# Optimization experiments

Measured on AMD Instinct MI355X. Metric: run time of the kernel, lower is better.

The kernel has to match this reference:

```python
import jax, jax.numpy as jnp
import numpy as np

N_NODES = 50000
N_EDGES = 800000
N_FEAT = 128
HIDDEN = 128
HEADS = 4
C = HIDDEN // HEADS  # per-head channels = 32
N_LAYERS = 3
OUT_DIM = 2048
N_GRAPHS = 1000
LEAKY = 0.2  # PyG GATConv default negative_slope


def setup_inputs() -> dict:
    key = jax.random.key(0)
    ks = jax.random.split(key, 12)
    x = jax.random.normal(ks[0], (N_NODES, N_FEAT), dtype=jnp.float32)
    edge_index = jax.random.randint(ks[1], (2, N_EDGES), 0, N_NODES, dtype=jnp.int32)
    edge_attr = jax.random.normal(ks[2], (N_EDGES, 1), dtype=jnp.float32)
    batch = (jnp.arange(N_NODES, dtype=jnp.int32) // (N_NODES // N_GRAPHS))  # 50 nodes per graph
    s = 1.0 / np.sqrt(HIDDEN)
    Ws = jax.random.normal(ks[3], (N_LAYERS, N_FEAT, HIDDEN), dtype=jnp.float32) * s
    att_src = jax.random.normal(ks[4], (N_LAYERS, HEADS, C), dtype=jnp.float32) * s
    att_dst = jax.random.normal(ks[5], (N_LAYERS, HEADS, C), dtype=jnp.float32) * s
    We = jax.random.normal(ks[6], (N_LAYERS, 1, HIDDEN), dtype=jnp.float32) * s
    att_e = jax.random.normal(ks[7], (N_LAYERS, HEADS, C), dtype=jnp.float32) * s
    biases = jnp.zeros((N_LAYERS, HIDDEN), dtype=jnp.float32)
    lin1_w = jax.random.normal(ks[8], (HIDDEN, OUT_DIM), dtype=jnp.float32) * s
    lin1_b = jnp.zeros((OUT_DIM,), dtype=jnp.float32)
    return {"x": x, "edge_index": edge_index, "edge_attr": edge_attr, "batch": batch,
            "Ws": Ws, "att_src": att_src, "att_dst": att_dst, "We": We,
            "att_e": att_e, "biases": biases, "lin1_w": lin1_w, "lin1_b": lin1_b}


def _gat_layer(x, src, dst, ea, W, a_s, a_d, We_l, a_e, b):
    """PyG GATConv: shared lin for src/dst, edge_dim=1, concat heads, eval mode."""
    N = x.shape[0]
    h = (x @ W).reshape(N, HEADS, C)                       # [N,H,C]
    al_s = jnp.einsum('nhc,hc->nh', h, a_s)                # [N,H]
    al_d = jnp.einsum('nhc,hc->nh', h, a_d)
    e = (ea @ We_l).reshape(-1, HEADS, C)                  # [E',H,C]
    al_e = jnp.einsum('ehc,hc->eh', e, a_e)
    logits = jax.nn.leaky_relu(al_s[src] + al_d[dst] + al_e, LEAKY)  # [E',H]
    # segment softmax over incoming edges of each dst node, per head
    m = jax.ops.segment_max(logits, dst, num_segments=N)
    m = jnp.where(jnp.isfinite(m), m, 0.0)
    ex = jnp.exp(logits - m[dst])
    den = jax.ops.segment_sum(ex, dst, num_segments=N)
    alpha = ex / (den[dst] + 1e-16)                        # [E',H]
    msg = alpha[:, :, None] * h[src]                       # [E',H,C]
    out = jax.ops.segment_sum(msg, dst, num_segments=N)    # [N,H,C]
    return out.reshape(N, HIDDEN) + b


def reference(x, edge_index, edge_attr, batch, Ws, att_src, att_dst, We, att_e, biases, lin1_w, lin1_b):
    N = x.shape[0]
    src, dst = edge_index[0], edge_index[1]
    # add_self_loops=True with fill_value='mean' (PyG default): self-loop
    # edge_attr at node i = mean of edge_attr over edges pointing to i.
    cnt = jax.ops.segment_sum(jnp.ones_like(edge_attr[:, 0]), dst, num_segments=N)
    ea_sum = jax.ops.segment_sum(edge_attr, dst, num_segments=N)
    ea_self = jnp.where(cnt[:, None] > 0, ea_sum / jnp.maximum(cnt[:, None], 1.0), 0.0)
    loop = jnp.arange(N, dtype=src.dtype)
    src_f = jnp.concatenate([src, loop])
    dst_f = jnp.concatenate([dst, loop])
    ea_f = jnp.concatenate([edge_attr, ea_self], axis=0)
    for l in range(N_LAYERS):
        x = _gat_layer(x, src_f, dst_f, ea_f, Ws[l], att_src[l], att_dst[l], We[l], att_e[l], biases[l])
        x = jax.nn.relu(x)  # dropout is identity in eval mode
    pooled = jax.ops.segment_max(x, batch, num_segments=N_GRAPHS, indices_are_sorted=True)
    out = pooled @ lin1_w + lin1_b
    return jax.nn.sigmoid(out)  # classes_is_bit=True
```

## Files before the change

kernel.cpp:

```cpp
#include <hip/hip_runtime.h>
#include <hip/hip_bf16.h>
#include <math.h>

#define NN 50000
#define NE 800000
#define HID 128
#define HEADS 4
#define CH 32
#define NG 1000
#define OUTD 2048
#define LEAKY 0.2f
#define NB196 ((NN + 255) / 256)

typedef __attribute__((ext_vector_type(8))) short bshort8;
typedef __attribute__((ext_vector_type(4))) float floatx4;

__device__ __forceinline__ float lrelu(float v) { return v >= 0.f ? v : LEAKY * v; }

__device__ __forceinline__ unsigned short f2bf(float f) {
    __hip_bfloat16 b = __float2bfloat16(f);
    return *reinterpret_cast<unsigned short*>(&b);
}
__device__ __forceinline__ float bflo(unsigned u) { return __uint_as_float(u << 16); }
__device__ __forceinline__ float bfhi(unsigned u) { return __uint_as_float(u & 0xffff0000u); }
__device__ __forceinline__ float bfu(unsigned short u) { return __uint_as_float(((unsigned)u) << 16); }

__global__ void k_hist(const int* __restrict__ ei, int* __restrict__ deg,
                       int* __restrict__ pos) {
    int e = blockIdx.x * 256 + threadIdx.x;
    if (e >= NE) return;
    pos[e] = atomicAdd(&deg[ei[NE + e]], 1);
}

__global__ __launch_bounds__(256) void k_s1(const int* __restrict__ deg,
                                            int* __restrict__ loc,
                                            int* __restrict__ bsum) {
    __shared__ int ws[4];
    int t = blockIdx.x * 256 + threadIdx.x;
    int lane = threadIdx.x & 63, wid = threadIdx.x >> 6;
    int v = (t < NN) ? deg[t] : 0;
    int run = v;
    for (int off = 1; off < 64; off <<= 1) {
        int u = __shfl_up(run, off);
        if (lane >= off) run += u;
    }
    if (lane == 63) ws[wid] = run;
    __syncthreads();
    int wadd = 0;
    if (wid > 0) wadd += ws[0];
    if (wid > 1) wadd += ws[1];
    if (wid > 2) wadd += ws[2];
    if (t < NN) loc[t] = run - v + wadd;
    if (threadIdx.x == 255) bsum[blockIdx.x] = wadd + run;
}

__global__ __launch_bounds__(256) void k_s2(const int* __restrict__ bsum,
                                            int* __restrict__ bexcl) {
    __shared__ int ws[4];
    int t = threadIdx.x;
    int lane = t & 63, wid = t >> 6;
    int v = (t < NB196) ? bsum[t] : 0;
    int run = v;
    for (int off = 1; off < 64; off <<= 1) {
        int u = __shfl_up(run, off);
        if (lane >= off) run += u;
    }
    if (lane == 63) ws[wid] = run;
    __syncthreads();
    int wadd = 0;
    if (wid > 0) wadd += ws[0];
    if (wid > 1) wadd += ws[1];
    if (wid > 2) wadd += ws[2];
    if (t < NB196) bexcl[t] = run - v + wadd;
}

__global__ __launch_bounds__(256) void k_s3(const int* __restrict__ loc,
                                            const int* __restrict__ bexcl,
                                            int* __restrict__ rowptr) {
    int t = blockIdx.x * 256 + threadIdx.x;
    if (t < NN) rowptr[t] = loc[t] + bexcl[blockIdx.x];
    if (t == 0) rowptr[NN] = NE;
}

__global__ void k_scatter(const int* __restrict__ ei, const float* __restrict__ ea,
                          const int* __restrict__ rowptr, const int* __restrict__ pos,
                          int2* __restrict__ ep) {
    int e = blockIdx.x * 256 + threadIdx.x;
    if (e >= NE) return;
    int d = ei[NE + e];
    int2 rec;
    rec.x = ei[e];
    rec.y = __float_as_int(ea[e]);
    ep[rowptr[d] + pos[e]] = rec;
}

__global__ void k_coef(const float* __restrict__ We, const float* __restrict__ att_e,
                       float* __restrict__ coef) {
    int t = threadIdx.x;
    if (t < 12) {
        int l = t >> 2, hh = t & 3;
        const float* w = We + l * HID + hh * CH;
        const float* a = att_e + l * HID + hh * CH;
        float s = 0.f;
        for (int c = 0; c < CH; ++c) s += w[c] * a[c];
        coef[t] = s;
    }
}

__global__ void k_xcvt(const float* __restrict__ X, unsigned short* __restrict__ Xb) {
    int t = blockIdx.x * 256 + threadIdx.x;
    if (t >= NN * HID / 4) return;
    float4 v = ((const float4*)X)[t];
    ushort4 o;
    o.x = f2bf(v.x); o.y = f2bf(v.y); o.z = f2bf(v.z); o.w = f2bf(v.w);
    ((ushort4*)Xb)[t] = o;
}

__global__ void k_wt(const float* __restrict__ Ws, unsigned short* __restrict__ Wt) {
    int t = blockIdx.x * 256 + threadIdx.x;
    if (t >= 3 * HID * HID) return;
    int l = t / (HID * HID), rem = t % (HID * HID);
    int k = rem >> 7, n = rem & 127;
    Wt[l * HID * HID + n * HID + k] = f2bf(Ws[l * HID * HID + k * HID + n]);
}

__global__ __launch_bounds__(256) void k_mm(const unsigned short* __restrict__ Xb,
                                            const unsigned short* __restrict__ Wt,
                                            unsigned short* __restrict__ H2) {
    int t = threadIdx.x;
    int wv = t >> 6, lane = t & 63;
    int m0 = blockIdx.x * 64 + wv * 16;
    int ln = lane & 15, kg = lane >> 4;
    int row = m0 + ln;
    int rc = row < NN ? row : NN - 1;
    floatx4 acc[8];
    #pragma unroll
    for (int nt = 0; nt < 8; ++nt) acc[nt] = (floatx4){0.f, 0.f, 0.f, 0.f};
    #pragma unroll
    for (int kc = 0; kc < HID; kc += 32) {
        bshort8 a = *(const bshort8*)&Xb[rc * HID + kc + kg * 8];
        #pragma unroll
        for (int nt = 0; nt < 8; ++nt) {
            bshort8 b = *(const bshort8*)&Wt[(nt * 16 + ln) * HID + kc + kg * 8];
            acc[nt] = __builtin_amdgcn_mfma_f32_16x16x32_bf16(a, b, acc[nt], 0, 0, 0);
        }
    }
    #pragma unroll
    for (int nt = 0; nt < 8; ++nt) {
        #pragma unroll
        for (int r = 0; r < 4; ++r) {
            int ro = m0 + kg * 4 + r;
            if (ro < NN) H2[ro * HID + nt * 16 + ln] = f2bf(acc[nt][r]);
        }
    }
}

__global__ void k_al(const unsigned short* __restrict__ H2,
                     const float* __restrict__ aw_s, const float* __restrict__ aw_d,
                     float* __restrict__ als, float* __restrict__ ald) {
    int t = blockIdx.x * 256 + threadIdx.x;
    if (t >= NN * HEADS) return;
    int n = t >> 2, h = t & 3;
    const unsigned* hw = (const unsigned*)(H2 + n * HID + h * CH);
    const float* sw = aw_s + h * CH;
    const float* dw = aw_d + h * CH;
    float s = 0.f, d = 0.f;
    #pragma unroll
    for (int i = 0; i < 16; ++i) {
        unsigned u = hw[i];
        float v0 = bflo(u), v1 = bfhi(u);
        s += v0 * sw[2 * i] + v1 * sw[2 * i + 1];
        d += v0 * dw[2 * i] + v1 * dw[2 * i + 1];
    }
    als[t] = s;
    ald[t] = d;
}

__global__ __launch_bounds__(256) void k_agg(const int* __restrict__ rowptr,
                                             const int2* __restrict__ ep,
                                             const float* __restrict__ als,
                                             const float* __restrict__ ald,
                                             const unsigned short* __restrict__ H2,
                                             const float* __restrict__ coef_l,
                                             const float* __restrict__ bias,
                                             unsigned short* __restrict__ xout) {
    int n = blockIdx.x * 4 + (threadIdx.x >> 6);
    if (n >= NN) return;
    int lane = threadIdx.x & 63;
    int c = lane * 2;
    int h = lane >> 4;
    const unsigned* H2w = (const unsigned*)H2;
    float coefh = coef_l[h];
    float aldh = ald[n * 4 + h];
    float s = 0.f, acc0 = 0.f, acc1 = 0.f, sum_ea = 0.f;
    int jb = rowptr[n], je = rowptr[n + 1];
    int j = jb;
    for (; j + 8 <= je; j += 8) {
        int2 e0 = ep[j],     e1 = ep[j + 1], e2 = ep[j + 2], e3 = ep[j + 3];
        int2 e4 = ep[j + 4], e5 = ep[j + 5], e6 = ep[j + 6], e7 = ep[j + 7];
        unsigned v0 = H2w[e0.x * 64 + lane];
        unsigned v1 = H2w[e1.x * 64 + lane];
        unsigned v2 = H2w[e2.x * 64 + lane];
        unsigned v3 = H2w[e3.x * 64 + lane];
        unsigned v4 = H2w[e4.x * 64 + lane];
        unsigned v5 = H2w[e5.x * 64 + lane];
        unsigned v6 = H2w[e6.x * 64 + lane];
        unsigned v7 = H2w[e7.x * 64 + lane];
        float l0 = als[e0.x * 4 + h], l1 = als[e1.x * 4 + h];
        float l2 = als[e2.x * 4 + h], l3 = als[e3.x * 4 + h];
        float l4 = als[e4.x * 4 + h], l5 = als[e5.x * 4 + h];
        float l6 = als[e6.x * 4 + h], l7 = als[e7.x * 4 + h];
        float a0 = __int_as_float(e0.y), a1 = __int_as_float(e1.y);
        float a2 = __int_as_float(e2.y), a3 = __int_as_float(e3.y);
        float a4 = __int_as_float(e4.y), a5 = __int_as_float(e5.y);
        float a6 = __int_as_float(e6.y), a7 = __int_as_float(e7.y);
        float p0 = __expf(lrelu(l0 + aldh + a0 * coefh));
        float p1 = __expf(lrelu(l1 + aldh + a1 * coefh));
        float p2 = __expf(lrelu(l2 + aldh + a2 * coefh));
        float p3 = __expf(lrelu(l3 + aldh + a3 * coefh));
        float p4 = __expf(lrelu(l4 + aldh + a4 * coefh));
        float p5 = __expf(lrelu(l5 + aldh + a5 * coefh));
        float p6 = __expf(lrelu(l6 + aldh + a6 * coefh));
        float p7 = __expf(lrelu(l7 + aldh + a7 * coefh));
        sum_ea += ((a0 + a1) + (a2 + a3)) + ((a4 + a5) + (a6 + a7));
        s += ((p0 + p1) + (p2 + p3)) + ((p4 + p5) + (p6 + p7));
        acc0 += p0 * bflo(v0) + p1 * bflo(v1);
        acc1 += p0 * bfhi(v0) + p1 * bfhi(v1);
        acc0 += p2 * bflo(v2) + p3 * bflo(v3);
        acc1 += p2 * bfhi(v2) + p3 * bfhi(v3);
        acc0 += p4 * bflo(v4) + p5 * bflo(v5);
        acc1 += p4 * bfhi(v4) + p5 * bfhi(v5);
        acc0 += p6 * bflo(v6) + p7 * bflo(v7);
        acc1 += p6 * bfhi(v6) + p7 * bfhi(v7);
    }
    for (; j < je; ++j) {
        int2 e0 = ep[j];
        float a0 = __int_as_float(e0.y);
        unsigned v0 = H2w[e0.x * 64 + lane];
        float p0 = __expf(lrelu(als[e0.x * 4 + h] + aldh + a0 * coefh));
        sum_ea += a0;
        s += p0;
        acc0 += p0 * bflo(v0);
        acc1 += p0 * bfhi(v0);
    }
    int degn = je - jb;
    float eaself = (degn > 0) ? sum_ea / (float)degn : 0.f;
    float ps = __expf(lrelu(als[n * 4 + h] + aldh + eaself * coefh));
    unsigned vs = H2w[n * 64 + lane];
    s += ps;
    acc0 += ps * bflo(vs);
    acc1 += ps * bfhi(vs);
    float inv = 1.0f / (s + 1e-16f);
    float o0 = fmaxf(acc0 * inv + bias[c], 0.f);
    float o1 = fmaxf(acc1 * inv + bias[c + 1], 0.f);
    ushort2 ov;
    ov.x = f2bf(o0);
    ov.y = f2bf(o1);
    *(ushort2*)&xout[n * HID + c] = ov;
}

__global__ void k_pool(const unsigned short* __restrict__ x, float* __restrict__ pooled) {
    int g = blockIdx.x;
    int c = threadIdx.x;
    float m = -INFINITY;
    const unsigned short* p = x + g * 50 * HID + c;
    for (int i = 0; i < 50; ++i) m = fmaxf(m, bfu(p[i * HID]));
    pooled[g * HID + c] = m;
}

__global__ __launch_bounds__(256) void k_out(const float* __restrict__ pooled,
                                             const float* __restrict__ W,
                                             const float* __restrict__ b,
                                             float* __restrict__ out) {
    __shared__ float sp[8][HID];
    int t = threadIdx.x;
    int o = blockIdx.x * 256 + t;
    int g0 = blockIdx.y * 8;
    for (int i = t; i < 8 * HID / 4; i += 256)
        ((float4*)sp)[i] = ((const float4*)(pooled + g0 * HID))[i];
    __syncthreads();
    float acc[8];
    #pragma unroll
    for (int g = 0; g < 8; ++g) acc[g] = 0.f;
    for (int k = 0; k < HID; ++k) {
        float wv = W[k * OUTD + o];
        #pragma unroll
        for (int g = 0; g < 8; ++g) acc[g] += sp[g][k] * wv;
    }
    float bb = b[o];
    #pragma unroll
    for (int g = 0; g < 8; ++g)
        out[(g0 + g) * OUTD + o] = 1.f / (1.f + expf(-(acc[g] + bb)));
}

extern "C" void kernel_launch(void* const* d_in, const int* in_sizes, int n_in,
                              void* d_out, int out_size, void* d_ws, size_t ws_size,
                              hipStream_t stream) {
    const float* x_in    = (const float*)d_in[0];
    const int*   ei      = (const int*)d_in[1];
    const float* ea      = (const float*)d_in[2];
    const float* Ws      = (const float*)d_in[4];
    const float* att_src = (const float*)d_in[5];
    const float* att_dst = (const float*)d_in[6];
    const float* We      = (const float*)d_in[7];
    const float* att_e   = (const float*)d_in[8];
    const float* biases  = (const float*)d_in[9];
    const float* lin1_w  = (const float*)d_in[10];
    const float* lin1_b  = (const float*)d_in[11];
    float* out = (float*)d_out;

    char* p = (char*)d_ws;
    int*   deg    = (int*)p;                 p += sizeof(int) * NN;
    int*   loc    = (int*)p;                 p += sizeof(int) * NN;
    int*   bsum   = (int*)p;                 p += sizeof(int) * 256;
    int*   bexcl  = (int*)p;                 p += sizeof(int) * 256;
    int*   rowptr = (int*)p;                 p += sizeof(int) * (NN + 1);
    p += sizeof(int) * 3;
    int*   pos    = (int*)p;                 p += sizeof(int) * NE;
    int2*  ep     = (int2*)p;                p += sizeof(int2) * NE;
    unsigned short* H2  = (unsigned short*)p; p += sizeof(short) * (size_t)NN * HID;
    unsigned short* Xb0 = (unsigned short*)p; p += sizeof(short) * (size_t)NN * HID;
    unsigned short* xa  = (unsigned short*)p; p += sizeof(short) * (size_t)NN * HID;
    unsigned short* xb  = (unsigned short*)p; p += sizeof(short) * (size_t)NN * HID;
    unsigned short* Wt  = (unsigned short*)p; p += sizeof(short) * 3 * HID * HID;
    float* als    = (float*)p;               p += sizeof(float) * NN * HEADS;
    float* ald    = (float*)p;               p += sizeof(float) * NN * HEADS;
    float* pooled = (float*)p;               p += sizeof(float) * NG * HID;
    float* coef   = (float*)p;               p += sizeof(float) * 12;

    hipMemsetAsync(deg, 0, sizeof(int) * NN, stream);
    k_hist<<<(NE + 255) / 256, 256, 0, stream>>>(ei, deg, pos);
    k_s1<<<NB196, 256, 0, stream>>>(deg, loc, bsum);
    k_s2<<<1, 256, 0, stream>>>(bsum, bexcl);
    k_s3<<<NB196, 256, 0, stream>>>(loc, bexcl, rowptr);
    k_scatter<<<(NE + 255) / 256, 256, 0, stream>>>(ei, ea, rowptr, pos, ep);
    k_coef<<<1, 64, 0, stream>>>(We, att_e, coef);
    k_wt<<<(3 * HID * HID + 255) / 256, 256, 0, stream>>>(Ws, Wt);
    k_xcvt<<<(NN * HID / 4 + 255) / 256, 256, 0, stream>>>(x_in, Xb0);

    for (int l = 0; l < 3; ++l) {
        const unsigned short* xin = (l == 0) ? Xb0 : (l == 1 ? xa : xb);
        unsigned short* xout      = (l == 1) ? xb : xa;
        k_mm<<<(NN + 63) / 64, 256, 0, stream>>>(xin, Wt + l * HID * HID, H2);
        k_al<<<(NN * HEADS + 255) / 256, 256, 0, stream>>>(
            H2, att_src + l * HEADS * CH, att_dst + l * HEADS * CH, als, ald);
        k_agg<<<NN / 4, 256, 0, stream>>>(rowptr, ep, als, ald,
                                          H2, coef + l * 4, biases + l * HID, xout);
    }
    k_pool<<<NG, HID, 0, stream>>>(xa, pooled);
    dim3 og(OUTD / 256, NG / 8);
    k_out<<<og, 256, 0, stream>>>(pooled, lin1_w, lin1_b, out);
}
```

Baseline: 435.5 us.

## Fuse attention logits into GEMM, pack edges to 32-bit, cooperative edge softmax

The per-node attention dot products move into the MFMA GEMM epilogue using cross-lane shuffle reductions, which removes the separate k_al kernel and its re-read of H2. Edge records shrink from int2 to one 32-bit word: a 16-bit source index plus a bf16 edge attribute. The aggregation kernel now spreads logit and exp work across lanes, one (edge, head) pair per lane over 16 edges at a time, and broadcasts the weights with readlane/bpermute. Before, every lane recomputed the logits for all edges. The costs are bf16 rounding of edge attributes, a source index that only fits because the node count is under 65536, and extra cross-lane traffic in the inner loop.

```diff
diff --git a/kernel.cpp b/kernel.cpp
--- a/kernel.cpp
+++ b/kernel.cpp
@@ -15,7 +15,7 @@
 typedef __attribute__((ext_vector_type(8))) short bshort8;
 typedef __attribute__((ext_vector_type(4))) float floatx4;
 
-__device__ __forceinline__ float lrelu(float v) { return v >= 0.f ? v : LEAKY * v; }
+__device__ __forceinline__ float lrelu(float v) { return fmaxf(v, LEAKY * v); }
 
 __device__ __forceinline__ unsigned short f2bf(float f) {
     __hip_bfloat16 b = __float2bfloat16(f);
@@ -84,13 +84,11 @@
 
 __global__ void k_scatter(const int* __restrict__ ei, const float* __restrict__ ea,
                           const int* __restrict__ rowptr, const int* __restrict__ pos,
-                          int2* __restrict__ ep) {
+                          unsigned* __restrict__ ep) {
     int e = blockIdx.x * 256 + threadIdx.x;
     if (e >= NE) return;
     int d = ei[NE + e];
-    int2 rec;
-    rec.x = ei[e];
-    rec.y = __float_as_int(ea[e]);
+    unsigned rec = (((unsigned)f2bf(ea[e])) << 16) | (unsigned)ei[e];
     ep[rowptr[d] + pos[e]] = rec;
 }
 
@@ -126,7 +124,11 @@
 
 __global__ __launch_bounds__(256) void k_mm(const unsigned short* __restrict__ Xb,
                                             const unsigned short* __restrict__ Wt,
-                                            unsigned short* __restrict__ H2) {
+                                            const float* __restrict__ aw_s,
+                                            const float* __restrict__ aw_d,
+                                            unsigned short* __restrict__ H2,
+                                            float* __restrict__ als,
+                                            float* __restrict__ ald) {
     int t = threadIdx.x;
     int wv = t >> 6, lane = t & 63;
     int m0 = blockIdx.x * 64 + wv * 16;
@@ -153,31 +155,50 @@
             if (ro < NN) H2[ro * HID + nt * 16 + ln] = f2bf(acc[nt][r]);
         }
     }
-}
-
-__global__ void k_al(const unsigned short* __restrict__ H2,
-                     const float* __restrict__ aw_s, const float* __restrict__ aw_d,
-                     float* __restrict__ als, float* __restrict__ ald) {
-    int t = blockIdx.x * 256 + threadIdx.x;
-    if (t >= NN * HEADS) return;
-    int n = t >> 2, h = t & 3;
-    const unsigned* hw = (const unsigned*)(H2 + n * HID + h * CH);
-    const float* sw = aw_s + h * CH;
-    const float* dw = aw_d + h * CH;
-    float s = 0.f, d = 0.f;
-    #pragma unroll
-    for (int i = 0; i < 16; ++i) {
-        unsigned u = hw[i];
-        float v0 = bflo(u), v1 = bfhi(u);
-        s += v0 * sw[2 * i] + v1 * sw[2 * i + 1];
-        d += v0 * dw[2 * i] + v1 * dw[2 * i + 1];
-    }
-    als[t] = s;
-    ald[t] = d;
+    float ws8[8], wd8[8];
+    #pragma unroll
+    for (int nt = 0; nt < 8; ++nt) {
+        ws8[nt] = aw_s[nt * 16 + ln];
+        wd8[nt] = aw_d[nt * 16 + ln];
+    }
+    float pas[4][4], pad[4][4];
+    #pragma unroll
+    for (int h = 0; h < 4; ++h) {
+        #pragma unroll
+        for (int r = 0; r < 4; ++r) {
+            pas[h][r] = acc[2 * h][r] * ws8[2 * h] + acc[2 * h + 1][r] * ws8[2 * h + 1];
+            pad[h][r] = acc[2 * h][r] * wd8[2 * h] + acc[2 * h + 1][r] * wd8[2 * h + 1];
+        }
+    }
+    #pragma unroll
+    for (int h = 0; h < 4; ++h) {
+        #pragma unroll
+        for (int r = 0; r < 4; ++r) {
+            #pragma unroll
+            for (int off = 1; off < 16; off <<= 1) {
+                pas[h][r] += __shfl_xor(pas[h][r], off);
+                pad[h][r] += __shfl_xor(pad[h][r], off);
+            }
+        }
+    }
+    if (ln < 4) {
+        #pragma unroll
+        for (int r = 0; r < 4; ++r) {
+            int ro = m0 + kg * 4 + r;
+            if (ro < NN) {
+                float vs = ln == 0 ? pas[0][r] : ln == 1 ? pas[1][r]
+                         : ln == 2 ? pas[2][r] : pas[3][r];
+                float vd = ln == 0 ? pad[0][r] : ln == 1 ? pad[1][r]
+                         : ln == 2 ? pad[2][r] : pad[3][r];
+                als[ro * 4 + ln] = vs;
+                ald[ro * 4 + ln] = vd;
+            }
+        }
+    }
 }
 
 __global__ __launch_bounds__(256) void k_agg(const int* __restrict__ rowptr,
-                                             const int2* __restrict__ ep,
+                                             const unsigned* __restrict__ ep,
                                              const float* __restrict__ als,
                                              const float* __restrict__ ald,
                                              const unsigned short* __restrict__ H2,
@@ -185,67 +206,70 @@
                                              const float* __restrict__ bias,
                                              unsigned short* __restrict__ xout) {
     int n = blockIdx.x * 4 + (threadIdx.x >> 6);
-    if (n >= NN) return;
     int lane = threadIdx.x & 63;
+    int hp1 = lane & 3;
+    int lq  = lane >> 2;
+    int hp2 = lane >> 4;
     int c = lane * 2;
-    int h = lane >> 4;
     const unsigned* H2w = (const unsigned*)H2;
-    float coefh = coef_l[h];
-    float aldh = ald[n * 4 + h];
-    float s = 0.f, acc0 = 0.f, acc1 = 0.f, sum_ea = 0.f;
+    float coef1 = coef_l[hp1];
+    float ald1 = ald[n * 4 + hp1];
+    float s = 0.f, acc0 = 0.f, acc1 = 0.f, ea4 = 0.f;
     int jb = rowptr[n], je = rowptr[n + 1];
-    int j = jb;
-    for (; j + 8 <= je; j += 8) {
-        int2 e0 = ep[j],     e1 = ep[j + 1], e2 = ep[j + 2], e3 = ep[j + 3];
-        int2 e4 = ep[j + 4], e5 = ep[j + 5], e6 = ep[j + 6], e7 = ep[j + 7];
-        unsigned v0 = H2w[e0.x * 64 + lane];
-        unsigned v1 = H2w[e1.x * 64 + lane];
-        unsigned v2 = H2w[e2.x * 64 + lane];
-        unsigned v3 = H2w[e3.x * 64 + lane];
-        unsigned v4 = H2w[e4.x * 64 + lane];
-        unsigned v5 = H2w[e5.x * 64 + lane];
-        unsigned v6 = H2w[e6.x * 64 + lane];
-        unsigned v7 = H2w[e7.x * 64 + lane];
-        float l0 = als[e0.x * 4 + h], l1 = als[e1.x * 4 + h];
-        float l2 = als[e2.x * 4 + h], l3 = als[e3.x * 4 + h];
-        float l4 = als[e4.x * 4 + h], l5 = als[e5.x * 4 + h];
-        float l6 = als[e6.x * 4 + h], l7 = als[e7.x * 4 + h];
-        float a0 = __int_as_float(e0.y), a1 = __int_as_float(e1.y);
-        float a2 = __int_as_float(e2.y), a3 = __int_as_float(e3.y);
-        float a4 = __int_as_float(e4.y), a5 = __int_as_float(e5.y);
-        float a6 = __int_as_float(e6.y), a7 = __int_as_float(e7.y);
-        float p0 = __expf(lrelu(l0 + aldh + a0 * coefh));
-        float p1 = __expf(lrelu(l1 + aldh + a1 * coefh));
-        float p2 = __expf(lrelu(l2 + aldh + a2 * coefh));
-        float p3 = __expf(lrelu(l3 + aldh + a3 * coefh));
-        float p4 = __expf(lrelu(l4 + aldh + a4 * coefh));
-        float p5 = __expf(lrelu(l5 + aldh + a5 * coefh));
-        float p6 = __expf(lrelu(l6 + aldh + a6 * coefh));
-        float p7 = __expf(lrelu(l7 + aldh + a7 * coefh));
-        sum_ea += ((a0 + a1) + (a2 + a3)) + ((a4 + a5) + (a6 + a7));
-        s += ((p0 + p1) + (p2 + p3)) + ((p4 + p5) + (p6 + p7));
-        acc0 += p0 * bflo(v0) + p1 * bflo(v1);
-        acc1 += p0 * bfhi(v0) + p1 * bfhi(v1);
-        acc0 += p2 * bflo(v2) + p3 * bflo(v3);
-        acc1 += p2 * bfhi(v2) + p3 * bfhi(v3);
-        acc0 += p4 * bflo(v4) + p5 * bflo(v5);
-        acc1 += p4 * bfhi(v4) + p5 * bfhi(v5);
-        acc0 += p6 * bflo(v6) + p7 * bflo(v7);
-        acc1 += p6 * bfhi(v6) + p7 * bfhi(v7);
-    }
-    for (; j < je; ++j) {
-        int2 e0 = ep[j];
-        float a0 = __int_as_float(e0.y);
-        unsigned v0 = H2w[e0.x * 64 + lane];
-        float p0 = __expf(lrelu(als[e0.x * 4 + h] + aldh + a0 * coefh));
-        sum_ea += a0;
-        s += p0;
-        acc0 += p0 * bflo(v0);
-        acc1 += p0 * bfhi(v0);
-    }
+    int j0 = jb;
+    for (; j0 + 16 <= je; j0 += 16) {
+        unsigned rec = ep[j0 + lq];
+        int srcp = rec & 0xffffu;
+        float a = __uint_as_float(rec & 0xffff0000u);
+        float p = __expf(lrelu(als[srcp * 4 + hp1] + ald1 + a * coef1));
+        ea4 += a;
+        float ps = p;
+        ps += __shfl_xor(ps, 4);  ps += __shfl_xor(ps, 8);
+        ps += __shfl_xor(ps, 16); ps += __shfl_xor(ps, 32);
+        s += __uint_as_float(__builtin_amdgcn_ds_bpermute(hp2 << 2, __float_as_int(ps)));
+        int pint = __float_as_int(p);
+        #pragma unroll
+        for (int k = 0; k < 16; ++k) {
+            int srck = __builtin_amdgcn_readlane(srcp, 4 * k);
+            float pk = __uint_as_float(
+                __builtin_amdgcn_ds_bpermute((hp2 << 2) + 16 * k, pint));
+            unsigned v = H2w[srck * 64 + lane];
+            acc0 += pk * bflo(v);
+            acc1 += pk * bfhi(v);
+        }
+    }
+    if (j0 < je) {
+        int eidx = j0 + lq;
+        bool val = eidx < je;
+        unsigned rec = val ? ep[eidx] : 0u;
+        int srcp = rec & 0xffffu;
+        float a = val ? __uint_as_float(rec & 0xffff0000u) : 0.f;
+        float p = val ? __expf(lrelu(als[srcp * 4 + hp1] + ald1 + a * coef1)) : 0.f;
+        ea4 += a;
+        float ps = p;
+        ps += __shfl_xor(ps, 4);  ps += __shfl_xor(ps, 8);
+        ps += __shfl_xor(ps, 16); ps += __shfl_xor(ps, 32);
+        s += __uint_as_float(__builtin_amdgcn_ds_bpermute(hp2 << 2, __float_as_int(ps)));
+        int pint = __float_as_int(p);
+        int nb = je - j0;
+        for (int k = 0; k < nb; ++k) {
+            int srck = __builtin_amdgcn_readlane(srcp, 4 * k);
+            float pk = __uint_as_float(
+                __builtin_amdgcn_ds_bpermute((hp2 << 2) + 16 * k, pint));
+            unsigned v = H2w[srck * 64 + lane];
+            acc0 += pk * bflo(v);
+            acc1 += pk * bfhi(v);
+        }
+    }
+    float easum = ea4;
+    easum += __shfl_xor(easum, 1);  easum += __shfl_xor(easum, 2);
+    easum += __shfl_xor(easum, 4);  easum += __shfl_xor(easum, 8);
+    easum += __shfl_xor(easum, 16); easum += __shfl_xor(easum, 32);
     int degn = je - jb;
-    float eaself = (degn > 0) ? sum_ea / (float)degn : 0.f;
-    float ps = __expf(lrelu(als[n * 4 + h] + aldh + eaself * coefh));
+    float eaself = (degn > 0) ? easum / (4.0f * (float)degn) : 0.f;
+    float coef2 = coef_l[hp2];
+    float ald2 = ald[n * 4 + hp2];
+    float ps = __expf(lrelu(als[n * 4 + hp2] + ald2 + eaself * coef2));
     unsigned vs = H2w[n * 64 + lane];
     s += ps;
     acc0 += ps * bflo(vs);
@@ -317,7 +341,7 @@
     int*   rowptr = (int*)p;                 p += sizeof(int) * (NN + 1);
     p += sizeof(int) * 3;
     int*   pos    = (int*)p;                 p += sizeof(int) * NE;
-    int2*  ep     = (int2*)p;                p += sizeof(int2) * NE;
+    unsigned* ep  = (unsigned*)p;            p += sizeof(unsigned) * NE;
     unsigned short* H2  = (unsigned short*)p; p += sizeof(short) * (size_t)NN * HID;
     unsigned short* Xb0 = (unsigned short*)p; p += sizeof(short) * (size_t)NN * HID;
     unsigned short* xa  = (unsigned short*)p; p += sizeof(short) * (size_t)NN * HID;
@@ -341,9 +365,10 @@
     for (int l = 0; l < 3; ++l) {
         const unsigned short* xin = (l == 0) ? Xb0 : (l == 1 ? xa : xb);
         unsigned short* xout      = (l == 1) ? xb : xa;
-        k_mm<<<(NN + 63) / 64, 256, 0, stream>>>(xin, Wt + l * HID * HID, H2);
-        k_al<<<(NN * HEADS + 255) / 256, 256, 0, stream>>>(
-            H2, att_src + l * HEADS * CH, att_dst + l * HEADS * CH, als, ald);
+        k_mm<<<(NN + 63) / 64, 256, 0, stream>>>(xin, Wt + l * HID * HID,
+                                                 att_src + l * HEADS * CH,
+                                                 att_dst + l * HEADS * CH,
+                                                 H2, als, ald);
         k_agg<<<NN / 4, 256, 0, stream>>>(rowptr, ep, als, ald,
                                           H2, coef + l * 4, biases + l * HID, xout);
     }
```

New measurement: 430.9 us. No clear change (-1.1%).
